# Optimization experiments

Measured on AMD Instinct MI355X. Metric: run time of the kernel, lower is better.

Reference implementation:

```python
import jax, jax.numpy as jnp
import numpy as np

RBF_START = 0.0
RBF_END = 8.0
RBF_STEPS = 32
OUT_SIZE = 64
ENERGY_SCALE = 0.01


def setup_inputs() -> dict:
    key = jax.random.key(0)
    k1, k2, k3, k4 = jax.random.split(key, 4)
    L, R = 512, 4096
    return {
        "lig_feat": jax.random.normal(k1, (L, RBF_STEPS, OUT_SIZE), dtype=jnp.float32),
        "rec_feat": jax.random.normal(k2, (R, RBF_STEPS, OUT_SIZE), dtype=jnp.float32),
        "lig_coord": jax.random.normal(k3, (L, 3), dtype=jnp.float32),
        "rec_coord": jax.random.normal(k4, (R, 3), dtype=jnp.float32),
    }


def reference(lig_feat, rec_feat, lig_coord, rec_coord):
    # attention coefficients: contract over (rbf step 'e' kept, feature 'f' summed)
    atn_coefs = jnp.einsum('lef,ref->lre', lig_feat, rec_feat)  # [L,R,steps]
    # pairwise distances [L,R]
    diff = lig_coord[:, None, :] - rec_coord[None, :, :]
    dists = jnp.sqrt(jnp.sum(diff * diff, axis=-1))
    # RBF encoding [L,R,steps]
    mu = jnp.linspace(RBF_START, RBF_END, RBF_STEPS, dtype=dists.dtype)
    sigma = (RBF_START - RBF_END) / RBF_STEPS
    z = (dists[..., None] - mu) / sigma
    rbfs = jnp.exp(-(z * z))
    # weighted energy sum (scalar)
    U = jnp.sum(atn_coefs * rbfs) * ENERGY_SCALE
    return U
```

## Files before the change

kernel.cpp:

```cpp
#include <hip/hip_runtime.h>
#include <math.h>

#define LN 512
#define RN 4096
#define EN 32
#define FN 64

#define BLT 128
#define BRT 128
#define EH  8

#define SQK      4.804489631554082f
#define MU_STEP  (8.0f / 31.0f)
#define SDLT     (SQK * MU_STEP)

typedef _Float16 half8 __attribute__((ext_vector_type(8)));
typedef __attribute__((ext_vector_type(4))) float f32x4;

#define BUFBYTES 32768
#define BPLANE   16384

#define WS_LIG 0
#define WS_REC (2u * 1024 * 1024)

#define LCHUNKS (LN * EN * 8)
#define RCHUNKS (RN * EN * 8)

typedef const __attribute__((address_space(1))) unsigned int* gas_ptr;
typedef __attribute__((address_space(3))) unsigned int* las_ptr;
#define GL16(g, l) __builtin_amdgcn_global_load_lds((gas_ptr)(g), (las_ptr)(l), 16, 0, 0)

__global__ __launch_bounds__(256) void ff_convert(
    const float* __restrict__ lig_feat, const float* __restrict__ rec_feat,
    unsigned short* __restrict__ lig_swz, unsigned short* __restrict__ rec_swz,
    float* __restrict__ out)
{
    if (blockIdx.x == 0 && threadIdx.x == 0) out[0] = 0.0f;

    int idx = blockIdx.x * 256 + threadIdx.x;
    const float* src;
    unsigned short* dst;
    if (idx < LCHUNKS) {
        src = lig_feat; dst = lig_swz;
    } else {
        idx -= LCHUNKS;
        src = rec_feat; dst = rec_swz;
    }
    const int row = idx >> 8;
    const int e   = (idx >> 3) & 31;
    const int gf  = idx & 7;

    const float* s = src + (((size_t)row * EN + e) * FN + gf * 8);
    const float4 v0 = *(const float4*)s;
    const float4 v1 = *(const float4*)(s + 4);

    const unsigned short q0 = __builtin_bit_cast(unsigned short, (_Float16)v0.x);
    const unsigned short q1 = __builtin_bit_cast(unsigned short, (_Float16)v0.y);
    const unsigned short q2 = __builtin_bit_cast(unsigned short, (_Float16)v0.z);
    const unsigned short q3 = __builtin_bit_cast(unsigned short, (_Float16)v0.w);
    const unsigned short q4 = __builtin_bit_cast(unsigned short, (_Float16)v1.x);
    const unsigned short q5 = __builtin_bit_cast(unsigned short, (_Float16)v1.y);
    const unsigned short q6 = __builtin_bit_cast(unsigned short, (_Float16)v1.z);
    const unsigned short q7 = __builtin_bit_cast(unsigned short, (_Float16)v1.w);
    uint4 o;
    o.x = (unsigned)q0 | ((unsigned)q1 << 16);
    o.y = (unsigned)q2 | ((unsigned)q3 << 16);
    o.z = (unsigned)q4 | ((unsigned)q5 << 16);
    o.w = (unsigned)q6 | ((unsigned)q7 << 16);

    const size_t dpos = (((size_t)row * EN + e) * 8 + (gf ^ (row & 7))) * 8;
    *(uint4*)(dst + dpos) = o;
}

__global__ __launch_bounds__(512, 1) void ff_mfma(
    const unsigned short* __restrict__ lig_swz,
    const unsigned short* __restrict__ rec_swz,
    const float* __restrict__ lig_coord,
    const float* __restrict__ rec_coord,
    float* __restrict__ out)
{
    __shared__ char lds[2 * BUFBYTES];

    const int tid  = threadIdx.x;
    const int lane = tid & 63;
    const int w    = tid >> 6;
    const int wl   = (w & 3) * 2;
    const int wr   = (w >> 2) * 4;
    const int lrow = lane & 15;
    const int lk   = lane >> 4;

    const int l0 = blockIdx.y * BLT;
    const int r0 = blockIdx.x * BRT;
    const int e0 = blockIdx.z * EH;

    int soff[2];
    #pragma unroll
    for (int k = 0; k < 2; ++k) {
        const int idx = k * 512 + tid;
        soff[k] = (idx >> 3) * (EN * 128) + (idx & 7) * 16;
    }
    const char* ligb = (const char*)lig_swz + (size_t)l0 * (EN * 128);
    const char* recb = (const char*)rec_swz + (size_t)r0 * (EN * 128);

#define STAGE(b, e_) do {                                                   \
        const int ebyte_ = (e_) * 128;                                      \
        _Pragma("unroll")                                                   \
        for (int k_ = 0; k_ < 2; ++k_) {                                    \
            const int idx_ = k_ * 512 + tid;                                \
            GL16(ligb + soff[k_] + ebyte_, lds + (b) * BUFBYTES + idx_ * 16);            \
            GL16(recb + soff[k_] + ebyte_, lds + (b) * BUFBYTES + BPLANE + idx_ * 16);   \
        }                                                                   \
    } while (0)

    float rcx[4], rcy[4], rcz[4];
    #pragma unroll
    for (int tj = 0; tj < 4; ++tj) {
        const int r = r0 + (wr + tj) * 16 + lrow;
        rcx[tj] = rec_coord[r * 3 + 0];
        rcy[tj] = rec_coord[r * 3 + 1];
        rcz[tj] = rec_coord[r * 3 + 2];
    }
    const float mu0s = -SQK * MU_STEP * (float)e0;
    float t[2][4][4];
    #pragma unroll
    for (int ti = 0; ti < 2; ++ti) {
        #pragma unroll
        for (int i = 0; i < 4; ++i) {
            const int l = l0 + (wl + ti) * 16 + lk * 4 + i;
            const float lx = lig_coord[l * 3 + 0];
            const float ly = lig_coord[l * 3 + 1];
            const float lz = lig_coord[l * 3 + 2];
            #pragma unroll
            for (int tj = 0; tj < 4; ++tj) {
                const float dx = lx - rcx[tj];
                const float dy = ly - rcy[tj];
                const float dz = lz - rcz[tj];
                const float d = sqrtf(fmaf(dx, dx, fmaf(dy, dy, dz * dz)));
                t[ti][tj][i] = fmaf(SQK, d, mu0s);
            }
        }
    }

    STAGE(0, e0);
    __syncthreads();

    float usum = 0.0f;

    for (int ee = 0; ee < EH; ++ee) {
        const int cur = ee & 1;
        const int e   = e0 + ee;

        if (ee + 1 < EH) STAGE(cur ^ 1, e + 1);

        const char* base = lds + cur * BUFBYTES;

        f32x4 acc[2][4];
        #pragma unroll
        for (int ti = 0; ti < 2; ++ti)
            #pragma unroll
            for (int tj = 0; tj < 4; ++tj)
                acc[ti][tj] = (f32x4){0.f, 0.f, 0.f, 0.f};

        #pragma unroll
        for (int kc = 0; kc < 2; ++kc) {
            const int inrow = (kc * 64 + lk * 16) ^ ((lrow & 7) << 4);
            half8 af[2], bf_[4];
            #pragma unroll
            for (int tt = 0; tt < 2; ++tt) {
                const int arow = (wl + tt) * 16 + lrow;
                af[tt] = *(const half8*)(base + arow * 128 + inrow);
            }
            #pragma unroll
            for (int tt = 0; tt < 4; ++tt) {
                const int brow = (wr + tt) * 16 + lrow;
                bf_[tt] = *(const half8*)(base + BPLANE + brow * 128 + inrow);
            }
            #pragma unroll
            for (int ti = 0; ti < 2; ++ti) {
                #pragma unroll
                for (int tj = 0; tj < 4; ++tj) {
                    acc[ti][tj] = __builtin_amdgcn_mfma_f32_16x16x32_f16(
                        af[ti], bf_[tj], acc[ti][tj], 0, 0, 0);
                }
            }
        }

        #pragma unroll
        for (int ti = 0; ti < 2; ++ti) {
            #pragma unroll
            for (int tj = 0; tj < 4; ++tj) {
                #pragma unroll
                for (int i = 0; i < 4; ++i) {
                    const float u = t[ti][tj][i] * t[ti][tj][i];
                    const float wgt = __builtin_amdgcn_exp2f(-u);
                    usum = fmaf(acc[ti][tj][i], wgt, usum);
                    t[ti][tj][i] -= SDLT;
                }
            }
        }

        __syncthreads();
    }

    float* red = (float*)lds;
    red[tid] = usum;
    __syncthreads();
    #pragma unroll
    for (int st = 256; st > 0; st >>= 1) {
        if (tid < st) red[tid] += red[tid + st];
        __syncthreads();
    }
    if (tid == 0) atomicAdd(out, red[0] * 0.01f);
#undef STAGE
}

extern "C" void kernel_launch(void* const* d_in, const int* in_sizes, int n_in,
                              void* d_out, int out_size, void* d_ws, size_t ws_size,
                              hipStream_t stream)
{
    const float* lig_feat  = (const float*)d_in[0];
    const float* rec_feat  = (const float*)d_in[1];
    const float* lig_coord = (const float*)d_in[2];
    const float* rec_coord = (const float*)d_in[3];
    float* out = (float*)d_out;

    unsigned short* lig_swz = (unsigned short*)((char*)d_ws + WS_LIG);
    unsigned short* rec_swz = (unsigned short*)((char*)d_ws + WS_REC);

    const int nChunks = LCHUNKS + RCHUNKS;
    ff_convert<<<nChunks / 256, 256, 0, stream>>>(lig_feat, rec_feat, lig_swz, rec_swz, out);

    const dim3 grid(RN / BRT, LN / BLT, EN / EH);
    ff_mfma<<<grid, dim3(512), 0, stream>>>(lig_swz, rec_swz, lig_coord, rec_coord, out);
}
```

Measured before the change: 36.93 us.

## Halve ligand tile and read ligand fragments directly from global memory

The ligand tile shrinks from 128 to 64 rows and the block from 512 to 256 threads, which doubles the grid. Ligand A-fragments are no longer staged through LDS. Each wave loads them directly from global memory in an unswizzled fp16 layout, so only the receptor plane is double-buffered in LDS. This halves LDS use per block and removes the ligand staging traffic, but ligand data now comes from global or L2 inside the MFMA loop without being hidden by the prefetch.

```diff
diff --git a/kernel.cpp b/kernel.cpp
--- a/kernel.cpp
+++ b/kernel.cpp
@@ -6,7 +6,7 @@
 #define EN 32
 #define FN 64
 
-#define BLT 128
+#define BLT 64
 #define BRT 128
 #define EH  8
 
@@ -17,8 +17,7 @@
 typedef _Float16 half8 __attribute__((ext_vector_type(8)));
 typedef __attribute__((ext_vector_type(4))) float f32x4;
 
-#define BUFBYTES 32768
-#define BPLANE   16384
+#define BUFBYTES 16384
 
 #define WS_LIG 0
 #define WS_REC (2u * 1024 * 1024)
@@ -32,7 +31,7 @@
 
 __global__ __launch_bounds__(256) void ff_convert(
     const float* __restrict__ lig_feat, const float* __restrict__ rec_feat,
-    unsigned short* __restrict__ lig_swz, unsigned short* __restrict__ rec_swz,
+    unsigned short* __restrict__ lig_h, unsigned short* __restrict__ rec_swz,
     float* __restrict__ out)
 {
     if (blockIdx.x == 0 && threadIdx.x == 0) out[0] = 0.0f;
@@ -40,11 +39,12 @@
     int idx = blockIdx.x * 256 + threadIdx.x;
     const float* src;
     unsigned short* dst;
+    int swz;
     if (idx < LCHUNKS) {
-        src = lig_feat; dst = lig_swz;
+        src = lig_feat; dst = lig_h; swz = 0;
     } else {
         idx -= LCHUNKS;
-        src = rec_feat; dst = rec_swz;
+        src = rec_feat; dst = rec_swz; swz = 1;
     }
     const int row = idx >> 8;
     const int e   = (idx >> 3) & 31;
@@ -68,12 +68,13 @@
     o.z = (unsigned)q4 | ((unsigned)q5 << 16);
     o.w = (unsigned)q6 | ((unsigned)q7 << 16);
 
-    const size_t dpos = (((size_t)row * EN + e) * 8 + (gf ^ (row & 7))) * 8;
+    const int gslot = swz ? (gf ^ (row & 7)) : gf;
+    const size_t dpos = (((size_t)row * EN + e) * 8 + gslot) * 8;
     *(uint4*)(dst + dpos) = o;
 }
 
-__global__ __launch_bounds__(512, 1) void ff_mfma(
-    const unsigned short* __restrict__ lig_swz,
+__global__ __launch_bounds__(256, 1) void ff_mfma(
+    const unsigned short* __restrict__ lig_h,
     const unsigned short* __restrict__ rec_swz,
     const float* __restrict__ lig_coord,
     const float* __restrict__ rec_coord,
@@ -84,8 +85,8 @@
     const int tid  = threadIdx.x;
     const int lane = tid & 63;
     const int w    = tid >> 6;
-    const int wl   = (w & 3) * 2;
-    const int wr   = (w >> 2) * 4;
+    const int wl   = (w & 1) * 2;
+    const int wr   = (w >> 1) * 4;
     const int lrow = lane & 15;
     const int lk   = lane >> 4;
 
@@ -93,22 +94,26 @@
     const int r0 = blockIdx.x * BRT;
     const int e0 = blockIdx.z * EH;
 
-    int soff[2];
-    #pragma unroll
-    for (int k = 0; k < 2; ++k) {
-        const int idx = k * 512 + tid;
+    int soff[4];
+    #pragma unroll
+    for (int k = 0; k < 4; ++k) {
+        const int idx = k * 256 + tid;
         soff[k] = (idx >> 3) * (EN * 128) + (idx & 7) * 16;
     }
-    const char* ligb = (const char*)lig_swz + (size_t)l0 * (EN * 128);
     const char* recb = (const char*)rec_swz + (size_t)r0 * (EN * 128);
+
+    const char* ligp = (const char*)lig_h;
+    int aoff[2];
+    #pragma unroll
+    for (int tt = 0; tt < 2; ++tt)
+        aoff[tt] = (l0 + (wl + tt) * 16 + lrow) * (EN * 128) + lk * 16;
 
 #define STAGE(b, e_) do {                                                   \
         const int ebyte_ = (e_) * 128;                                      \
         _Pragma("unroll")                                                   \
-        for (int k_ = 0; k_ < 2; ++k_) {                                    \
-            const int idx_ = k_ * 512 + tid;                                \
-            GL16(ligb + soff[k_] + ebyte_, lds + (b) * BUFBYTES + idx_ * 16);            \
-            GL16(recb + soff[k_] + ebyte_, lds + (b) * BUFBYTES + BPLANE + idx_ * 16);   \
+        for (int k_ = 0; k_ < 4; ++k_) {                                    \
+            const int idx_ = k_ * 256 + tid;                                \
+            GL16(recb + soff[k_] + ebyte_, lds + (b) * BUFBYTES + idx_ * 16); \
         }                                                                   \
     } while (0)
 
@@ -120,7 +125,7 @@
         rcy[tj] = rec_coord[r * 3 + 1];
         rcz[tj] = rec_coord[r * 3 + 2];
     }
-    const float mu0s = -SQK * MU_STEP * (float)e0;
+    const float mu0s = -SDLT * (float)e0;
     float t[2][4][4];
     #pragma unroll
     for (int ti = 0; ti < 2; ++ti) {
@@ -153,6 +158,7 @@
         if (ee + 1 < EH) STAGE(cur ^ 1, e + 1);
 
         const char* base = lds + cur * BUFBYTES;
+        const int ebyte = e * 128;
 
         f32x4 acc[2][4];
         #pragma unroll
@@ -166,14 +172,12 @@
             const int inrow = (kc * 64 + lk * 16) ^ ((lrow & 7) << 4);
             half8 af[2], bf_[4];
             #pragma unroll
-            for (int tt = 0; tt < 2; ++tt) {
-                const int arow = (wl + tt) * 16 + lrow;
-                af[tt] = *(const half8*)(base + arow * 128 + inrow);
-            }
+            for (int tt = 0; tt < 2; ++tt)
+                af[tt] = *(const half8*)(ligp + aoff[tt] + ebyte + kc * 64);
             #pragma unroll
             for (int tt = 0; tt < 4; ++tt) {
                 const int brow = (wr + tt) * 16 + lrow;
-                bf_[tt] = *(const half8*)(base + BPLANE + brow * 128 + inrow);
+                bf_[tt] = *(const half8*)(base + brow * 128 + inrow);
             }
             #pragma unroll
             for (int ti = 0; ti < 2; ++ti) {
@@ -206,7 +210,7 @@
     red[tid] = usum;
     __syncthreads();
     #pragma unroll
-    for (int st = 256; st > 0; st >>= 1) {
+    for (int st = 128; st > 0; st >>= 1) {
         if (tid < st) red[tid] += red[tid + st];
         __syncthreads();
     }
@@ -224,12 +228,12 @@
     const float* rec_coord = (const float*)d_in[3];
     float* out = (float*)d_out;
 
-    unsigned short* lig_swz = (unsigned short*)((char*)d_ws + WS_LIG);
+    unsigned short* lig_h   = (unsigned short*)((char*)d_ws + WS_LIG);
     unsigned short* rec_swz = (unsigned short*)((char*)d_ws + WS_REC);
 
     const int nChunks = LCHUNKS + RCHUNKS;
-    ff_convert<<<nChunks / 256, 256, 0, stream>>>(lig_feat, rec_feat, lig_swz, rec_swz, out);
+    ff_convert<<<nChunks / 256, 256, 0, stream>>>(lig_feat, rec_feat, lig_h, rec_swz, out);
 
     const dim3 grid(RN / BRT, LN / BLT, EN / EH);
-    ff_mfma<<<grid, dim3(512), 0, stream>>>(lig_swz, rec_swz, lig_coord, rec_coord, out);
+    ff_mfma<<<grid, dim3(256), 0, stream>>>(lig_h, rec_swz, lig_coord, rec_coord, out);
 }
```

Result: slower. 43.66 us (+18.2%).
